# Performance work log

Measured on AMD Instinct MI355X. Metric: run time of the kernel, lower is better.

The kernel has to match this reference:

```python
import jax, jax.numpy as jnp
import numpy as np

B, T1, T2 = 4, 768, 256
T = T1 + T2            # n_token
NI = T2                # n_i_token
D = 1024               # n_embd
H_MLP = 4096           # n_mlp_hidden
L = 12                 # n_layer
V = 512                # num_class / vocab_size
EPS = 1e-5


def _ln(x, g, b):
    m = jnp.mean(x, axis=-1, keepdims=True)
    v = jnp.mean((x - m) ** 2, axis=-1, keepdims=True)
    return (x - m) * jax.lax.rsqrt(v + EPS) * g + b


def setup_inputs() -> dict:
    key = jax.random.key(0)
    ks = jax.random.split(key, 16)
    s = 0.02
    return {
        "xt": jax.random.randint(ks[0], (B, T1), 0, V, dtype=jnp.int32),
        "zi": jax.random.randint(ks[1], (B, T2), 0, V, dtype=jnp.int32),
        "pos_emb": jax.random.normal(ks[2], (T, D), jnp.float32) * s,
        "t_emb": jax.random.normal(ks[3], (V, D), jnp.float32) * s,
        "i_emb": jax.random.normal(ks[4], (V, D), jnp.float32) * s,
        "ln1_g": jnp.ones((L, D), jnp.float32),
        "ln1_b": jnp.zeros((L, D), jnp.float32),
        "Wq": jax.random.normal(ks[5], (L, D, D), jnp.float32) * s,
        "Wk": jax.random.normal(ks[6], (L, D, D), jnp.float32) * s,
        "Wv": jax.random.normal(ks[7], (L, D, D), jnp.float32) * s,
        "ln2_g": jnp.ones((L, D), jnp.float32),
        "ln2_b": jnp.zeros((L, D), jnp.float32),
        "W1": jax.random.normal(ks[8], (L, D, H_MLP), jnp.float32) * s,
        "b1": jnp.zeros((L, H_MLP), jnp.float32),
        "W2": jax.random.normal(ks[9], (L, H_MLP, D), jnp.float32) * s,
        "b2": jnp.zeros((L, D), jnp.float32),
        "ro_W": jax.random.normal(ks[10], (D, V), jnp.float32) * s,
        "ro_b": jnp.zeros((V,), jnp.float32),
    }


def reference(xt, zi, pos_emb, t_emb, i_emb, ln1_g, ln1_b, Wq, Wk, Wv,
              ln2_g, ln2_b, W1, b1, W2, b2, ro_W, ro_b):
    # token + position embeddings: [B, T, D]
    H0 = jnp.concatenate([i_emb[zi], t_emb[xt]], axis=1) + pos_emb[None]
    scale = 1.0 / np.sqrt(D).astype(np.float32)

    def layer(H, p):
        g1, b1_, wq, wk, wv, g2, b2_, w1, bb1, w2, bb2 = p
        H1 = _ln(H, g1, b1_)
        q = H1 @ wq  # [B, T, D]
        k = H1 @ wk
        v = H1 @ wv
        attn = jax.nn.softmax(jnp.einsum('bid,bjd->bij', q, k) * scale, axis=-1)
        H = H + jnp.einsum('bij,bjd->bid', attn, v)
        # second application with extra rescale by embedding dim (H.shape[2] == D)
        H = H + jnp.einsum('bij,bjd->bid', attn / D, v)
        H2 = _ln(H, g2, b2_)
        H = H + jax.nn.gelu(H2 @ w1 + bb1, approximate=False) @ w2 + bb2
        return H, None

    params = (ln1_g, ln1_b, Wq, Wk, Wv, ln2_g, ln2_b, W1, b1, W2, b2)
    H, _ = jax.lax.scan(layer, H0, params)
    prediction = H @ ro_W + ro_b  # [B, T, V]
    return prediction[:, NI:, :]
```

## Files before the change

### kernel.cpp

```cpp
#include <hip/hip_runtime.h>
#include <hip/hip_bf16.h>
#include <math.h>

#define D_EMB  1024
#define T_TOK  1024
#define T1_TOK 768
#define T2_TOK 256
#define HMLP   4096
#define NLAYER 12
#define VCLS   512

typedef __attribute__((ext_vector_type(8))) short          short8;
typedef __attribute__((ext_vector_type(4))) float          f32x4;
typedef __attribute__((ext_vector_type(4))) unsigned short us4;

__device__ __forceinline__ unsigned short f2bf(float f) {
    union { float f; unsigned int u; } c; c.f = f;
    unsigned int u = c.u;
    return (unsigned short)((u + 0x7FFFu + ((u >> 16) & 1u)) >> 16);
}

__device__ __forceinline__ void gld_lds16(const unsigned short* g, unsigned short* l) {
    __builtin_amdgcn_global_load_lds(
        (__attribute__((address_space(1))) void*)g,
        (__attribute__((address_space(3))) void*)l, 16, 0, 0);
}

__global__ __launch_bounds__(256)
void embed_kernel(const int* __restrict__ xt, const int* __restrict__ zi,
                  const float* __restrict__ pos, const float* __restrict__ temb,
                  const float* __restrict__ iemb, float* __restrict__ H)
{
    const long idx = (long)blockIdx.x * 256 + threadIdx.x;
    const long e   = idx * 4;
    const int  dd  = (int)(e & (D_EMB - 1));
    const long bt  = e >> 10;
    const int  t   = (int)(bt & (T_TOK - 1));
    const int  b   = (int)(bt >> 10);
    const float* src;
    if (t < T2_TOK) src = iemb + (long)zi[b * T2_TOK + t] * D_EMB + dd;
    else            src = temb + (long)xt[b * T1_TOK + (t - T2_TOK)] * D_EMB + dd;
    float4 sv = *(const float4*)src;
    float4 pv = *(const float4*)(pos + (long)t * D_EMB + dd);
    float4 o; o.x = sv.x + pv.x; o.y = sv.y + pv.y; o.z = sv.z + pv.z; o.w = sv.w + pv.w;
    *(float4*)(H + e) = o;
}

__global__ __launch_bounds__(256)
void ln_kernel(const float* __restrict__ X, const float* __restrict__ g,
               const float* __restrict__ b, unsigned short* __restrict__ Y)
{
    const long row = blockIdx.x;
    const int  tid = threadIdx.x;
    float4 v = *(const float4*)(X + row * D_EMB + tid * 4);
    float s = v.x + v.y + v.z + v.w;
    float q = v.x*v.x + v.y*v.y + v.z*v.z + v.w*v.w;
    #pragma unroll
    for (int o = 32; o >= 1; o >>= 1) { s += __shfl_down(s, o); q += __shfl_down(q, o); }
    __shared__ float rs[4], rq[4];
    const int w = tid >> 6;
    if ((tid & 63) == 0) { rs[w] = s; rq[w] = q; }
    __syncthreads();
    s = rs[0] + rs[1] + rs[2] + rs[3];
    q = rq[0] + rq[1] + rq[2] + rq[3];
    const float mean = s * (1.0f / D_EMB);
    const float var  = q * (1.0f / D_EMB) - mean * mean;
    const float rstd = rsqrtf(var + 1e-5f);
    float4 gg = *(const float4*)(g + tid * 4);
    float4 bb = *(const float4*)(b + tid * 4);
    us4 o;
    o.x = f2bf((v.x - mean) * rstd * gg.x + bb.x);
    o.y = f2bf((v.y - mean) * rstd * gg.y + bb.y);
    o.z = f2bf((v.z - mean) * rstd * gg.z + bb.z);
    o.w = f2bf((v.w - mean) * rstd * gg.w + bb.w);
    *(us4*)(Y + row * D_EMB + tid * 4) = o;
}

__global__ __launch_bounds__(256)
void softmax_kernel(const float* __restrict__ S, unsigned short* __restrict__ P)
{
    const long row = blockIdx.x;
    const int  tid = threadIdx.x;
    float4 v = *(const float4*)(S + row * T_TOK + tid * 4);
    const float sc = 0.03125f;
    float a = v.x * sc, b = v.y * sc, c = v.z * sc, d = v.w * sc;
    float mx = fmaxf(fmaxf(a, b), fmaxf(c, d));
    #pragma unroll
    for (int o = 32; o >= 1; o >>= 1) mx = fmaxf(mx, __shfl_down(mx, o));
    __shared__ float rm[4], rsum[4];
    const int w = tid >> 6;
    if ((tid & 63) == 0) rm[w] = mx;
    __syncthreads();
    mx = fmaxf(fmaxf(rm[0], rm[1]), fmaxf(rm[2], rm[3]));
    float e0 = expf(a - mx), e1 = expf(b - mx), e2 = expf(c - mx), e3 = expf(d - mx);
    float s = e0 + e1 + e2 + e3;
    #pragma unroll
    for (int o = 32; o >= 1; o >>= 1) s += __shfl_down(s, o);
    if ((tid & 63) == 0) rsum[w] = s;
    __syncthreads();
    s = rsum[0] + rsum[1] + rsum[2] + rsum[3];
    const float inv = 1.0f / s;
    us4 o4; o4.x = f2bf(e0 * inv); o4.y = f2bf(e1 * inv);
    o4.z = f2bf(e2 * inv); o4.w = f2bf(e3 * inv);
    *(us4*)(P + row * T_TOK + tid * 4) = o4;
}

__global__ __launch_bounds__(256)
void convT_kernel(const float* __restrict__ src, unsigned short* __restrict__ dst,
                  int K, int N)
{
    __shared__ unsigned short tile[32][33];
    const int tn = blockIdx.x, tk = blockIdx.y;
    const int tx = threadIdx.x & 31, ty = threadIdx.x >> 5;
    #pragma unroll
    for (int i = 0; i < 4; ++i) {
        const int r = ty + i * 8;
        tile[r][tx] = f2bf(src[(long)(tk * 32 + r) * N + tn * 32 + tx]);
    }
    __syncthreads();
    #pragma unroll
    for (int i = 0; i < 4; ++i) {
        const int r = ty + i * 8;
        dst[(long)(tn * 32 + r) * K + tk * 32 + tx] = tile[tx][r];
    }
}

__global__ __launch_bounds__(256)
void wconv_kernel(const float* __restrict__ Wq, const float* __restrict__ Wk,
                  const float* __restrict__ Wv, const float* __restrict__ W1,
                  const float* __restrict__ W2,
                  unsigned short* __restrict__ WqT, unsigned short* __restrict__ WkT,
                  unsigned short* __restrict__ WvT, unsigned short* __restrict__ W1T,
                  unsigned short* __restrict__ W2T)
{
    __shared__ unsigned short tile[32][33];
    const int t = blockIdx.x;
    const float* src; unsigned short* dst; int K, N, tk, tn;
    if (t < 3072) {
        const int wsel = t >> 10, tt = t & 1023;
        src = (wsel == 0) ? Wq : (wsel == 1) ? Wk : Wv;
        dst = (wsel == 0) ? WqT : (wsel == 1) ? WkT : WvT;
        K = 1024; N = 1024; tn = tt & 31; tk = tt >> 5;
    } else if (t < 7168) {
        const int tt = t - 3072;
        src = W1; dst = W1T; K = 1024; N = 4096; tn = tt & 127; tk = tt >> 7;
    } else {
        const int tt = t - 7168;
        src = W2; dst = W2T; K = 4096; N = 1024; tn = tt & 31; tk = tt >> 5;
    }
    const int tx = threadIdx.x & 31, ty = threadIdx.x >> 5;
    #pragma unroll
    for (int i = 0; i < 4; ++i) {
        const int r = ty + i * 8;
        tile[r][tx] = f2bf(src[(long)(tk * 32 + r) * N + tn * 32 + tx]);
    }
    __syncthreads();
    #pragma unroll
    for (int i = 0; i < 4; ++i) {
        const int r = ty + i * 8;
        dst[(long)(tn * 32 + r) * K + tk * 32 + tx] = tile[tx][r];
    }
}

__global__ __launch_bounds__(256)
void cvt_bf16_kernel(const float* __restrict__ X, unsigned short* __restrict__ Y)
{
    const long i = ((long)blockIdx.x * 256 + threadIdx.x) * 4;
    float4 v = *(const float4*)(X + i);
    us4 o; o.x = f2bf(v.x); o.y = f2bf(v.y); o.z = f2bf(v.z); o.w = f2bf(v.w);
    *(us4*)(Y + i) = o;
}

template<int EPI, int TN>
__global__ __launch_bounds__(256)
void gemm_bt(const unsigned short* __restrict__ A,
             const unsigned short* __restrict__ B0,
             const unsigned short* __restrict__ B1,
             const unsigned short* __restrict__ B2,
             void* __restrict__ C0, void* __restrict__ C1, void* __restrict__ C2,
             const float* __restrict__ bias,
             int M, int N, int K, int kLen,
             long sAz, long sBz, long sCz, float alpha)
{
    constexpr int FN = TN / 32;
    constexpr int ABUF = 128 * 32;
    constexpr int BBUF = TN * 32;
    __shared__ unsigned short As[2 * ABUF];
    __shared__ unsigned short Bs[2 * BBUF];

    const int z = blockIdx.z;
    const unsigned short* Ap = A + (long)z * sAz;
    const unsigned short* Bp = (B1 != nullptr) ? (z == 0 ? B0 : (z == 1 ? B1 : B2))
                                               : B0 + (long)z * sBz;
    void* Cp = (C1 != nullptr) ? (z == 0 ? C0 : (z == 1 ? C1 : C2)) : C0;
    const long czoff = (C1 != nullptr) ? 0 : (long)z * sCz;

    const int gx = gridDim.x, gy = gridDim.y;
    const int o  = blockIdx.x + gx * blockIdx.y;
    const int nwg = gx * gy;
    const int virt = (nwg & 7) ? o : ((o & 7) * (nwg >> 3) + (o >> 3));
    const int ntile = virt / gy;
    int mtile = virt - ntile * gy;
    if constexpr (EPI == 4) mtile = (mtile / 6) * 8 + 2 + (mtile % 6);
    const int m0 = mtile * 128, n0 = ntile * TN;
    const int kOff = (kLen < K) ? z * kLen : 0;

    const int tid = threadIdx.x;
    const int l = tid & 63, w = tid >> 6;
    const int wm = (w >> 1) * 64, wn = (w & 1) * (TN / 2);
    const int lr = l & 15, hi = l >> 4;

    const int r0 = tid >> 2;
    const int s0 = (tid & 3) ^ ((r0 >> 1) & 3);
    const unsigned short* gA0 = Ap + (long)(m0 + r0) * K + kOff + s0 * 8;
    const unsigned short* gA1 = Ap + (long)(m0 + r0 + 64) * K + kOff + s0 * 8;
    const unsigned short* gB0 = Bp + (long)(n0 + r0) * K + kOff + s0 * 8;
    const unsigned short* gB1 = (TN == 128) ? Bp + (long)(n0 + r0 + 64) * K + kOff + s0 * 8
                                            : nullptr;
    const int lA0 = w * 512, lA1 = 2048 + w * 512;
    const int lB0 = w * 512, lB1 = 2048 + w * 512;

    f32x4 acc[4][FN];
    #pragma unroll
    for (int f = 0; f < 4; ++f)
        #pragma unroll
        for (int gq = 0; gq < FN; ++gq)
            acc[f][gq] = (f32x4){0.f, 0.f, 0.f, 0.f};

    const int nk = kLen >> 5;
    gld_lds16(gA0, As + lA0);
    gld_lds16(gA1, As + lA1);
    gld_lds16(gB0, Bs + lB0);
    if constexpr (TN == 128) gld_lds16(gB1, Bs + lB1);
    __syncthreads();

    for (int t = 0; t < nk; ++t) {
        const int cur = t & 1;
        const int aB = (cur ^ 1) * ABUF, bB = (cur ^ 1) * BBUF;
        if (t + 1 < nk) {
            const int k1 = (t + 1) << 5;
            gld_lds16(gA0 + k1, As + aB + lA0);
            gld_lds16(gA1 + k1, As + aB + lA1);
            gld_lds16(gB0 + k1, Bs + bB + lB0);
            if constexpr (TN == 128) gld_lds16(gB1 + k1, Bs + bB + lB1);
        }
        const int aC = cur * ABUF, bC = cur * BBUF;
        short8 af[4], bg[FN];
        #pragma unroll
        for (int f = 0; f < 4; ++f) {
            const int rr = wm + f * 16 + lr;
            const int sl = hi ^ ((rr >> 1) & 3);
            af[f] = *(const short8*)&As[aC + rr * 32 + sl * 8];
        }
        #pragma unroll
        for (int gq = 0; gq < FN; ++gq) {
            const int rn = wn + gq * 16 + lr;
            const int sl = hi ^ ((rn >> 1) & 3);
            bg[gq] = *(const short8*)&Bs[bC + rn * 32 + sl * 8];
        }
        #pragma unroll
        for (int f = 0; f < 4; ++f)
            #pragma unroll
            for (int gq = 0; gq < FN; ++gq)
                acc[f][gq] = __builtin_amdgcn_mfma_f32_16x16x32_bf16(
                    af[f], bg[gq], acc[f][gq], 0, 0, 0);
        __syncthreads();
    }

    #pragma unroll
    for (int f = 0; f < 4; ++f) {
        #pragma unroll
        for (int gq = 0; gq < FN; ++gq) {
            const int gm0 = m0 + wm + f * 16 + hi * 4;
            const int gn  = n0 + wn + gq * 16 + lr;
            if constexpr (EPI == 7) {
                if (z == 2) {
                    us4 ov;
                    ov.x = f2bf(acc[f][gq][0]); ov.y = f2bf(acc[f][gq][1]);
                    ov.z = f2bf(acc[f][gq][2]); ov.w = f2bf(acc[f][gq][3]);
                    const long idx = (long)(gm0 >> 10) * (T_TOK * D_EMB)
                                   + (long)gn * T_TOK + (gm0 & (T_TOK - 1));
                    *(us4*)&((unsigned short*)Cp)[idx] = ov;
                    continue;
                }
            }
            #pragma unroll
            for (int r = 0; r < 4; ++r) {
                const int gm = gm0 + r;
                float v = acc[f][gq][r];
                if constexpr (EPI == 0) {
                    ((float*)Cp)[czoff + (long)gm * N + gn] = v;
                } else if constexpr (EPI == 1) {
                    v += bias[gn];
                    const float ge = 0.5f * v * (1.0f + erff(v * 0.70710678118f));
                    ((unsigned short*)Cp)[(long)gm * N + gn] = f2bf(ge);
                } else if constexpr (EPI == 3) {
                    float* c = (float*)Cp + czoff + (long)gm * N + gn;
                    *c = *c + alpha * v;
                } else if constexpr (EPI == 4) {
                    const int tt = gm & (T_TOK - 1);
                    ((float*)Cp)[(long)((gm >> 10) * T1_TOK + (tt - T2_TOK)) * VCLS + gn]
                        = v + bias[gn];
                } else if constexpr (EPI == 5 || EPI == 7) {
                    ((unsigned short*)Cp)[(long)gm * N + gn] = f2bf(v);
                } else if constexpr (EPI == 6) {
                    atomicAdd((float*)Cp + (long)gm * N + gn,
                              v + ((z == 0) ? bias[gn] : 0.f));
                }
            }
        }
    }
}

extern "C" void kernel_launch(void* const* d_in, const int* in_sizes, int n_in,
                              void* d_out, int out_size, void* d_ws, size_t ws_size,
                              hipStream_t stream)
{
    (void)in_sizes; (void)n_in; (void)out_size; (void)ws_size;
    const int*   xt   = (const int*)d_in[0];
    const int*   zi   = (const int*)d_in[1];
    const float* pos  = (const float*)d_in[2];
    const float* temb = (const float*)d_in[3];
    const float* iemb = (const float*)d_in[4];
    const float* ln1g = (const float*)d_in[5];
    const float* ln1b = (const float*)d_in[6];
    const float* Wq   = (const float*)d_in[7];
    const float* Wk   = (const float*)d_in[8];
    const float* Wv   = (const float*)d_in[9];
    const float* ln2g = (const float*)d_in[10];
    const float* ln2b = (const float*)d_in[11];
    const float* W1   = (const float*)d_in[12];
    const float* b1   = (const float*)d_in[13];
    const float* W2   = (const float*)d_in[14];
    const float* b2   = (const float*)d_in[15];
    const float* roW  = (const float*)d_in[16];
    const float* rob  = (const float*)d_in[17];
    float* out = (float*)d_out;

    char* wsb = (char*)d_ws;
    float*          H    = (float*)(wsb + 0);
    unsigned short* LNb  = (unsigned short*)(wsb + 16777216);
    float*          S    = (float*)(wsb + 25165824);
    unsigned short* Qb   = (unsigned short*)(wsb + 41943040);
    unsigned short* Kb   = (unsigned short*)(wsb + 50331648);
    unsigned short* VT   = (unsigned short*)(wsb + 58720256);
    unsigned short* Pb   = (unsigned short*)(wsb + 67108864);
    unsigned short* Hid  = (unsigned short*)(wsb + 41943040);
    unsigned short* WqT  = (unsigned short*)(wsb + 75497472);
    unsigned short* WkT  = (unsigned short*)(wsb + 77594624);
    unsigned short* WvT  = (unsigned short*)(wsb + 79691776);
    unsigned short* W1T  = (unsigned short*)(wsb + 81788928);
    unsigned short* W2T  = (unsigned short*)(wsb + 90177536);
    unsigned short* roWT = W1T;
    unsigned short* Hbf  = LNb;

    const long TD = (long)T_TOK * D_EMB;
    const long TT = (long)T_TOK * T_TOK;

    embed_kernel<<<4096, 256, 0, stream>>>(xt, zi, pos, temb, iemb, H);

    for (int lyr = 0; lyr < NLAYER; ++lyr) {
        const long dd = (long)lyr * D_EMB * D_EMB;
        const long d1 = (long)lyr * D_EMB * HMLP;
        wconv_kernel<<<11264, 256, 0, stream>>>(
            Wq + dd, Wk + dd, Wv + dd, W1 + d1, W2 + d1,
            WqT, WkT, WvT, W1T, W2T);
        ln_kernel<<<4096, 256, 0, stream>>>(H, ln1g + lyr * D_EMB, ln1b + lyr * D_EMB, LNb);
        gemm_bt<7, 128><<<dim3(8, 32, 3), 256, 0, stream>>>(
            LNb, WqT, WkT, WvT, Qb, Kb, VT, nullptr,
            4096, D_EMB, D_EMB, D_EMB, 0L, 0L, 0L, 1.f);
        gemm_bt<0, 64><<<dim3(16, 8, 4), 256, 0, stream>>>(
            Qb, Kb, nullptr, nullptr, S, nullptr, nullptr, nullptr,
            T_TOK, T_TOK, D_EMB, D_EMB, TD, TD, TT, 1.f);
        softmax_kernel<<<4096, 256, 0, stream>>>(S, Pb);
        gemm_bt<3, 64><<<dim3(16, 8, 4), 256, 0, stream>>>(
            Pb, VT, nullptr, nullptr, H, nullptr, nullptr, nullptr,
            T_TOK, D_EMB, T_TOK, T_TOK, TT, TD, TD, 1.0f + 1.0f / (float)D_EMB);
        ln_kernel<<<4096, 256, 0, stream>>>(H, ln2g + lyr * D_EMB, ln2b + lyr * D_EMB, LNb);
        gemm_bt<1, 128><<<dim3(32, 32, 1), 256, 0, stream>>>(
            LNb, W1T, nullptr, nullptr, Hid, nullptr, nullptr, b1 + (long)lyr * HMLP,
            4096, HMLP, D_EMB, D_EMB, 0L, 0L, 0L, 1.f);
        gemm_bt<6, 128><<<dim3(8, 32, 2), 256, 0, stream>>>(
            Hid, W2T, nullptr, nullptr, H, nullptr, nullptr, b2 + (long)lyr * D_EMB,
            4096, D_EMB, HMLP, HMLP / 2, 0L, 0L, 0L, 1.f);
    }
    cvt_bf16_kernel<<<4096, 256, 0, stream>>>(H, Hbf);
    convT_kernel<<<dim3(16, 32), 256, 0, stream>>>(roW, roWT, D_EMB, VCLS);
    gemm_bt<4, 64><<<dim3(8, 24, 1), 256, 0, stream>>>(
        Hbf, roWT, nullptr, nullptr, out, nullptr, nullptr, rob,
        4096, VCLS, D_EMB, D_EMB, 0L, 0L, 0L, 1.f);
}
```

Before: 3.111 ms.

## Triple-buffer GEMM LDS pipeline and vectorize weight transpose-convert

The GEMM main loop moves from double to triple buffering. Global-to-LDS loads for tile t+2 are issued while tile t is computed, and the full __syncthreads is replaced with explicit vmcnt waits plus raw s_barrier, so two tiles of loads stay in flight. The weight transpose/convert kernel switches from 32x32 tiles with scalar loads to 64x64 tiles using float4 loads and 4-wide bf16 stores, cutting its block count by four. The cost is more LDS per GEMM block, which may lower occupancy, and the hand-counted vmcnt values depend on the number of loads issued per stage.

After: 3.198 ms. 2.8% more time.

```diff
diff --git a/kernel.cpp b/kernel.cpp
--- a/kernel.cpp
+++ b/kernel.cpp
@@ -133,32 +133,42 @@
                   unsigned short* __restrict__ WvT, unsigned short* __restrict__ W1T,
                   unsigned short* __restrict__ W2T)
 {
-    __shared__ unsigned short tile[32][33];
+    __shared__ unsigned short tile[64][66];
     const int t = blockIdx.x;
     const float* src; unsigned short* dst; int K, N, tk, tn;
-    if (t < 3072) {
-        const int wsel = t >> 10, tt = t & 1023;
+    if (t < 768) {
+        const int wsel = t >> 8, tt = t & 255;
         src = (wsel == 0) ? Wq : (wsel == 1) ? Wk : Wv;
         dst = (wsel == 0) ? WqT : (wsel == 1) ? WkT : WvT;
-        K = 1024; N = 1024; tn = tt & 31; tk = tt >> 5;
-    } else if (t < 7168) {
-        const int tt = t - 3072;
-        src = W1; dst = W1T; K = 1024; N = 4096; tn = tt & 127; tk = tt >> 7;
+        K = 1024; N = 1024; tk = tt >> 4; tn = tt & 15;
+    } else if (t < 1792) {
+        const int tt = t - 768;
+        src = W1; dst = W1T; K = 1024; N = 4096; tk = tt >> 6; tn = tt & 63;
     } else {
-        const int tt = t - 7168;
-        src = W2; dst = W2T; K = 4096; N = 1024; tn = tt & 31; tk = tt >> 5;
-    }
-    const int tx = threadIdx.x & 31, ty = threadIdx.x >> 5;
+        const int tt = t - 1792;
+        src = W2; dst = W2T; K = 4096; N = 1024; tk = tt >> 4; tn = tt & 15;
+    }
+    const int r  = threadIdx.x >> 4;
+    const int c4 = threadIdx.x & 15;
     #pragma unroll
     for (int i = 0; i < 4; ++i) {
-        const int r = ty + i * 8;
-        tile[r][tx] = f2bf(src[(long)(tk * 32 + r) * N + tn * 32 + tx]);
+        const int row = r + i * 16;
+        float4 v = *(const float4*)(src + (long)(tk * 64 + row) * N + tn * 64 + c4 * 4);
+        tile[row][c4 * 4 + 0] = f2bf(v.x);
+        tile[row][c4 * 4 + 1] = f2bf(v.y);
+        tile[row][c4 * 4 + 2] = f2bf(v.z);
+        tile[row][c4 * 4 + 3] = f2bf(v.w);
     }
     __syncthreads();
     #pragma unroll
     for (int i = 0; i < 4; ++i) {
-        const int r = ty + i * 8;
-        dst[(long)(tn * 32 + r) * K + tk * 32 + tx] = tile[tx][r];
+        const int rr = r + i * 16;
+        us4 o;
+        o.x = tile[c4 * 4 + 0][rr];
+        o.y = tile[c4 * 4 + 1][rr];
+        o.z = tile[c4 * 4 + 2][rr];
+        o.w = tile[c4 * 4 + 3][rr];
+        *(us4*)(dst + (long)(tn * 64 + rr) * K + tk * 64 + c4 * 4) = o;
     }
 }
 
@@ -185,8 +195,8 @@
     constexpr int FN = TN / 32;
     constexpr int ABUF = 128 * 32;
     constexpr int BBUF = TN * 32;
-    __shared__ unsigned short As[2 * ABUF];
-    __shared__ unsigned short Bs[2 * BBUF];
+    __shared__ unsigned short As[3 * ABUF];
+    __shared__ unsigned short Bs[3 * BBUF];
 
     const int z = blockIdx.z;
     const unsigned short* Ap = A + (long)z * sAz;
@@ -228,22 +238,28 @@
             acc[f][gq] = (f32x4){0.f, 0.f, 0.f, 0.f};
 
     const int nk = kLen >> 5;
-    gld_lds16(gA0, As + lA0);
-    gld_lds16(gA1, As + lA1);
-    gld_lds16(gB0, Bs + lB0);
-    if constexpr (TN == 128) gld_lds16(gB1, Bs + lB1);
-    __syncthreads();
+    auto STAGE = [&](int t, int buf) {
+        const int k = t << 5;
+        gld_lds16(gA0 + k, As + buf * ABUF + lA0);
+        gld_lds16(gA1 + k, As + buf * ABUF + lA1);
+        gld_lds16(gB0 + k, Bs + buf * BBUF + lB0);
+        if constexpr (TN == 128) gld_lds16(gB1 + k, Bs + buf * BBUF + lB1);
+    };
+
+    STAGE(0, 0);
+    if (nk > 1) {
+        STAGE(1, 1);
+        if constexpr (TN == 128) asm volatile("s_waitcnt vmcnt(4)" ::: "memory");
+        else                     asm volatile("s_waitcnt vmcnt(3)" ::: "memory");
+    } else {
+        asm volatile("s_waitcnt vmcnt(0)" ::: "memory");
+    }
+    __builtin_amdgcn_s_barrier();
+    __builtin_amdgcn_sched_barrier(0);
 
     for (int t = 0; t < nk; ++t) {
-        const int cur = t & 1;
-        const int aB = (cur ^ 1) * ABUF, bB = (cur ^ 1) * BBUF;
-        if (t + 1 < nk) {
-            const int k1 = (t + 1) << 5;
-            gld_lds16(gA0 + k1, As + aB + lA0);
-            gld_lds16(gA1 + k1, As + aB + lA1);
-            gld_lds16(gB0 + k1, Bs + bB + lB0);
-            if constexpr (TN == 128) gld_lds16(gB1 + k1, Bs + bB + lB1);
-        }
+        const int cur = t % 3;
+        if (t + 2 < nk) STAGE(t + 2, (t + 2) % 3);
         const int aC = cur * ABUF, bC = cur * BBUF;
         short8 af[4], bg[FN];
         #pragma unroll
@@ -264,7 +280,15 @@
             for (int gq = 0; gq < FN; ++gq)
                 acc[f][gq] = __builtin_amdgcn_mfma_f32_16x16x32_bf16(
                     af[f], bg[gq], acc[f][gq], 0, 0, 0);
-        __syncthreads();
+        __builtin_amdgcn_sched_barrier(0);
+        if (t + 2 < nk) {
+            if constexpr (TN == 128) asm volatile("s_waitcnt vmcnt(4)" ::: "memory");
+            else                     asm volatile("s_waitcnt vmcnt(3)" ::: "memory");
+        } else if (t + 1 < nk) {
+            asm volatile("s_waitcnt vmcnt(0)" ::: "memory");
+        }
+        __builtin_amdgcn_s_barrier();
+        __builtin_amdgcn_sched_barrier(0);
     }
 
     #pragma unroll
@@ -362,7 +386,7 @@
     for (int lyr = 0; lyr < NLAYER; ++lyr) {
         const long dd = (long)lyr * D_EMB * D_EMB;
         const long d1 = (long)lyr * D_EMB * HMLP;
-        wconv_kernel<<<11264, 256, 0, stream>>>(
+        wconv_kernel<<<2816, 256, 0, stream>>>(
             Wq + dd, Wk + dd, Wv + dd, W1 + d1, W2 + d1,
             WqT, WkT, WvT, W1T, W2T);
         ln_kernel<<<4096, 256, 0, stream>>>(H, ln1g + lyr * D_EMB, ln1b + lyr * D_EMB, LNb);
```
